# Kernel tuning notes

Hardware: AMD Instinct MI355X
Metric: run time of the kernel (lower is better)

Reference implementation:

```python
import jax, jax.numpy as jnp
import numpy as np
import math

T, C = 8192, 1024

def setup_inputs() -> dict:
    key = jax.random.key(0)
    ks = jax.random.split(key, 10)
    s = 1.0 / math.sqrt(C)
    return {
        "x": jax.random.normal(ks[0], (T, C), dtype=jnp.float32),
        "Wq": jax.random.normal(ks[1], (C, C), dtype=jnp.float32) * s,
        "bq": jax.random.normal(ks[2], (C,), dtype=jnp.float32) * s,
        "Wk": jax.random.normal(ks[3], (C, C), dtype=jnp.float32) * s,
        "bk": jax.random.normal(ks[4], (C,), dtype=jnp.float32) * s,
        "Wv": jax.random.normal(ks[5], (C, C), dtype=jnp.float32) * s,
        "bv": jax.random.normal(ks[6], (C,), dtype=jnp.float32) * s,
        "Wp": jax.random.normal(ks[7], (C, C), dtype=jnp.float32) * s,
        "bp": jax.random.normal(ks[8], (C,), dtype=jnp.float32) * s,
    }

def reference(x, Wq, bq, Wk, bk, Wv, bv, Wp, bp):
    # Single-head causal self-attention over an unbatched (T, C) sequence.
    t, c = x.shape
    q = x @ Wq.T + bq          # (T, C)
    k = x @ Wk.T + bk          # (T, C)
    v = x @ Wv.T + bv          # (T, C)
    att = (q @ k.T) / math.sqrt(c)                      # (T, T)
    causal = jnp.tril(jnp.ones((t, t), dtype=bool))
    att = jnp.where(causal, att, -jnp.inf)
    att = jax.nn.softmax(att, axis=-1)
    y = att @ v                                         # (T, C)
    y = y @ Wp.T + bp
    return y
```

## Files before the change

### kernel.cpp

```cpp
#include <hip/hip_runtime.h>
#include <hip/hip_bf16.h>

typedef __bf16 bf16x8 __attribute__((ext_vector_type(8)));
typedef float f32x4 __attribute__((ext_vector_type(4)));

static constexpr int Tn = 8192;
static constexpr int Cn = 1024;

#define DEVI __device__ __forceinline__

DEVI float bf2f(ushort u) { union { uint i; float f; } c; c.i = ((uint)u) << 16; return c.f; }
DEVI ushort f2bf(float f) {
  uint x = __builtin_bit_cast(uint, f);
  x += 0x7fffu + ((x >> 16) & 1u);
  return (ushort)(x >> 16);
}

typedef const __attribute__((address_space(1))) void glb_v;
typedef __attribute__((address_space(3))) void lds_v;

#define BAR()   __builtin_amdgcn_s_barrier()
#define SCH0()  __builtin_amdgcn_sched_barrier(0)
#define PRIO1() __builtin_amdgcn_s_setprio(1)
#define PRIO0() __builtin_amdgcn_s_setprio(0)

__global__ __launch_bounds__(256) void cast_all(
    const float* __restrict__ x, const float* __restrict__ wq, const float* __restrict__ wk,
    const float* __restrict__ wv, const float* __restrict__ wp,
    const float* __restrict__ bq, const float* __restrict__ bk, const float* __restrict__ bv,
    ushort* __restrict__ xb, ushort* __restrict__ wqkv, ushort* __restrict__ wpb,
    float* __restrict__ bqkv, float* __restrict__ lsum)
{
  const long long NX = (long long)Tn * Cn;
  const long long NW = (long long)Cn * Cn;
  if (blockIdx.x == 12291) {
    float4 z; z.x = z.y = z.z = z.w = 0.f;
#pragma unroll
    for (int j = 0; j < 8; ++j) ((float4*)lsum)[threadIdx.x * 8 + j] = z;
    return;
  }
  if (blockIdx.x >= 12288) {
    int id = ((blockIdx.x - 12288) * 256 + threadIdx.x) * 4;
#pragma unroll
    for (int e = 0; e < 4; ++e) {
      int j = id + e;
      if (j < 3 * Cn) bqkv[j] = j < Cn ? bq[j] : (j < 2 * Cn ? bk[j - Cn] : bv[j - 2 * Cn]);
    }
    return;
  }
  long long i = ((long long)blockIdx.x * 256 + threadIdx.x) * 4;
  const float* src; ushort* dst; long long off;
  if (i < NX) { src = x; dst = xb; off = i; }
  else {
    long long r = i - NX; int seg = (int)(r >> 20); off = r & (NW - 1);
    if (seg < 3) { src = seg == 0 ? wq : seg == 1 ? wk : wv; dst = wqkv + (size_t)seg * NW; }
    else         { src = wp; dst = wpb; }
  }
  float4 v = *reinterpret_cast<const float4*>(src + off);
  ushort4 o; o.x = f2bf(v.x); o.y = f2bf(v.y); o.z = f2bf(v.z); o.w = f2bf(v.w);
  *reinterpret_cast<ushort4*>(dst + off) = o;
}

template<bool OUT_BF16, bool HAS_BIAS, bool QKT, bool PVM, bool SPLIT3>
__global__ __launch_bounds__(256, 2)
void gemm_rp(const ushort* __restrict__ A, const ushort* __restrict__ Bt,
             const float* __restrict__ bias, void* __restrict__ outp,
             float* __restrict__ lsum,
             int K, int lda, int ldb, int ldc, float scale)
{
  __shared__ __align__(16) ushort sm[32768];

  const int tid = threadIdx.x, lane = tid & 63, wid = tid >> 6;
  const int wm = wid >> 1, wn = wid & 1;
  const int ln15 = lane & 15, lsec = lane >> 4;

  const int bx = blockIdx.x;
  int by = blockIdx.y;
  if (QKT && by < bx) return;
  if (PVM) by = (int)gridDim.y - 1 - by;
  const int rowA0 = by * 128, col0 = bx * 128;
  int NT = K >> 6;
  if (PVM) { int kl = (by + 1) * 128; if (kl < K) NT = kl >> 6; }

  const uint smb = (uint)(uintptr_t)&sm[0];

  auto stage = [&](int t, int b) {
    const int tt = t < NT ? t : NT - 1;
    const size_t k0 = (size_t)(tt << 6);
#pragma unroll
    for (int i = 0; i < 4; ++i) {
      int s = tid + i * 256; int row = s >> 3; int kcs = (s & 7) ^ (row & 7);
      const ushort* g = A + (size_t)(rowA0 + row) * (size_t)lda + k0 + kcs * 8;
      __builtin_amdgcn_global_load_lds((glb_v*)g, (lds_v*)(&sm[b * 16384 + s * 8]), 16, 0, 0);
    }
#pragma unroll
    for (int i = 0; i < 4; ++i) {
      int s = tid + i * 256; int row = s >> 3; int kcs = (s & 7) ^ (row & 7);
      const ushort* g = Bt + (size_t)(col0 + row) * (size_t)ldb + k0 + kcs * 8;
      __builtin_amdgcn_global_load_lds((glb_v*)g, (lds_v*)(&sm[b * 16384 + 8192 + s * 8]), 16, 0, 0);
    }
  };

  uint offA[2][4], offB[2][4];
#pragma unroll
  for (int ks = 0; ks < 2; ++ks) {
    int kc = ks * 4 + lsec;
#pragma unroll
    for (int mi = 0; mi < 4; ++mi) {
      int r = wm * 64 + mi * 16 + ln15;
      offA[ks][mi] = (uint)((r * 64 + (kc ^ (r & 7)) * 8) * 2);
    }
#pragma unroll
    for (int ni = 0; ni < 4; ++ni) {
      int c = wn * 64 + ni * 16 + ln15;
      offB[ks][ni] = (uint)(16384 + (c * 64 + (kc ^ (c & 7)) * 8) * 2);
    }
  }

  bf16x8 f0A[4], f0B[4], f1A[4], f1B[4];
  f32x4 acc[4][4] = {};

#define DSR(d, a) asm volatile("ds_read_b128 %0, %1" : "=v"(d) : "v"(a))
#define MMAC(FA, FB) { _Pragma("unroll") for (int mi = 0; mi < 4; ++mi) \
    _Pragma("unroll") for (int ni = 0; ni < 4; ++ni) \
      acc[mi][ni] = __builtin_amdgcn_mfma_f32_16x16x32_bf16(FA[mi], FB[ni], acc[mi][ni], 0, 0, 0); }

  stage(0, 0); stage(1, 1);
  asm volatile("s_waitcnt vmcnt(8)" ::: "memory");
  BAR();
  SCH0();
#pragma unroll
  for (int mi = 0; mi < 4; ++mi) DSR(f0A[mi], smb + offA[0][mi]);
#pragma unroll
  for (int ni = 0; ni < 4; ++ni) DSR(f0B[ni], smb + offB[0][ni]);
  SCH0();

  uint boff = 0;
  for (int t = 0; t < NT; ++t, boff ^= 32768u) {
#pragma unroll
    for (int mi = 0; mi < 4; ++mi) DSR(f1A[mi], smb + boff + offA[1][mi]);
#pragma unroll
    for (int ni = 0; ni < 4; ++ni) DSR(f1B[ni], smb + boff + offB[1][ni]);
    SCH0();
    asm volatile("s_waitcnt lgkmcnt(8)" ::: "memory");
    SCH0();
    PRIO1(); MMAC(f0A, f0B); PRIO0();
    SCH0();
    asm volatile("s_waitcnt lgkmcnt(0)" ::: "memory");
    BAR();
    stage(t + 2, t & 1);
    SCH0();
    asm volatile("s_waitcnt vmcnt(8)" ::: "memory");
    BAR();
    SCH0();
    const uint bo1 = boff ^ 32768u;
#pragma unroll
    for (int mi = 0; mi < 4; ++mi) DSR(f0A[mi], smb + bo1 + offA[0][mi]);
#pragma unroll
    for (int ni = 0; ni < 4; ++ni) DSR(f0B[ni], smb + bo1 + offB[0][ni]);
    SCH0();
    PRIO1(); MMAC(f1A, f1B); PRIO0();
    SCH0();
  }
  asm volatile("s_waitcnt vmcnt(0) lgkmcnt(0)" ::: "memory");
#undef DSR
#undef MMAC

  if constexpr (QKT) {
#pragma unroll
    for (int mi = 0; mi < 4; ++mi) {
#pragma unroll
      for (int j = 0; j < 4; ++j) {
        const int row = rowA0 + wm * 64 + mi * 16 + lsec * 4 + j;
        float rs = 0.f;
        ushort pb[4];
#pragma unroll
        for (int ni = 0; ni < 4; ++ni) {
          const int col = col0 + wn * 64 + ni * 16 + ln15;
          float p = 0.f;
          if (col <= row) p = __expf(acc[mi][ni][j] * scale);
          pb[ni] = f2bf(p);
          rs += bf2f(pb[ni]);
        }
#pragma unroll
        for (int o = 1; o < 16; o <<= 1) rs += __shfl_xor(rs, o);
        if (ln15 == 0) atomicAdd(&lsum[row], rs);
#pragma unroll
        for (int ni = 0; ni < 4; ++ni) {
          const int col = col0 + wn * 64 + ni * 16 + ln15;
          ((ushort*)outp)[(size_t)row * (size_t)ldc + col] = pb[ni];
        }
      }
    }
  } else {
#pragma unroll
    for (int mi = 0; mi < 4; ++mi) {
#pragma unroll
      for (int j = 0; j < 4; ++j) {
        const int row = rowA0 + wm * 64 + mi * 16 + lsec * 4 + j;
        float inv = 1.f;
        if constexpr (PVM) inv = 1.0f / lsum[row];
#pragma unroll
        for (int ni = 0; ni < 4; ++ni) {
          const int colg = col0 + wn * 64 + ni * 16 + ln15;
          float val = acc[mi][ni][j] * scale;
          if constexpr (PVM) val *= inv;
          if constexpr (HAS_BIAS) val += bias[colg];
          int col = colg; size_t segoff = 0;
          if constexpr (SPLIT3) { int seg = colg >> 10; col = colg & 1023; segoff = (size_t)seg * (size_t)Tn * Cn; }
          if constexpr (OUT_BF16) ((ushort*)outp)[segoff + (size_t)row * (size_t)ldc + col] = f2bf(val);
          else                    ((float*)outp)[segoff + (size_t)row * (size_t)ldc + col] = val;
        }
      }
    }
  }
}

__global__ __launch_bounds__(256) void transpose64(const ushort* __restrict__ in,
                                                   ushort* __restrict__ out,
                                                   int ldin, int ldout)
{
  __shared__ ushort tile[64][65];
  const int c0 = blockIdx.x * 64, r0 = blockIdx.y * 64;
  const int t = threadIdx.x;
#pragma unroll
  for (int i = t; i < 512; i += 256) {
    int r = i >> 3, kc = i & 7;
    uint4 v = *reinterpret_cast<const uint4*>(in + (size_t)(r0 + r) * ldin + c0 + kc * 8);
    const ushort* u = reinterpret_cast<const ushort*>(&v);
#pragma unroll
    for (int j = 0; j < 8; ++j) tile[r][kc * 8 + j] = u[j];
  }
  __syncthreads();
#pragma unroll
  for (int i = t; i < 512; i += 256) {
    int c = i >> 3, rc = i & 7;
    union { uint4 v; ushort u[8]; } pk;
#pragma unroll
    for (int j = 0; j < 8; ++j) pk.u[j] = tile[rc * 8 + j][c];
    *reinterpret_cast<uint4*>(out + (size_t)(c0 + c) * ldout + r0 + rc * 8) = pk.v;
  }
}

extern "C" void kernel_launch(void* const* d_in, const int* in_sizes, int n_in,
                              void* d_out, int out_size, void* d_ws, size_t ws_size,
                              hipStream_t stream)
{
  (void)in_sizes; (void)n_in; (void)out_size; (void)ws_size;
  const float* x  = (const float*)d_in[0];
  const float* Wq = (const float*)d_in[1];
  const float* bq = (const float*)d_in[2];
  const float* Wk = (const float*)d_in[3];
  const float* bk = (const float*)d_in[4];
  const float* Wv = (const float*)d_in[5];
  const float* bv = (const float*)d_in[6];
  const float* Wp = (const float*)d_in[7];
  const float* bp = (const float*)d_in[8];

  char* w = (char*)d_ws;
  const size_t TC = (size_t)Tn * Cn * 2, CC = (size_t)Cn * Cn * 2;
  ushort* xb   = (ushort*)w; w += TC;
  ushort* Wqkv = (ushort*)w; w += 3 * CC;
  ushort* wpb  = (ushort*)w; w += CC;
  float*  bqkv = (float*)w;  w += 16384;
  float*  lsum = (float*)w;  w += 32768;
  ushort* Qb   = (ushort*)w; w += TC;
  ushort* Kb   = (ushort*)w; w += TC;
  ushort* Vb   = (ushort*)w; w += TC;
  ushort* Vt   = (ushort*)w; w += TC;
  ushort* Yb   = (ushort*)w; w += TC;
  ushort* S    = (ushort*)w; w += (size_t)Tn * Tn * 2;

  cast_all<<<12292, 256, 0, stream>>>(x, Wq, Wk, Wv, Wp, bq, bk, bv,
                                      xb, Wqkv, wpb, bqkv, lsum);

  gemm_rp<true, true, false, false, true><<<dim3(24, 64), 256, 0, stream>>>(
      xb, Wqkv, bqkv, Qb, nullptr, Cn, Cn, Cn, Cn, 1.0f);

  transpose64<<<dim3(Cn / 64, Tn / 64), 256, 0, stream>>>(Vb, Vt, Cn, Tn);

  gemm_rp<true, false, true, false, false><<<dim3(64, 64), 256, 0, stream>>>(
      Qb, Kb, nullptr, S, lsum, Cn, Cn, Cn, Tn, 0.03125f);

  gemm_rp<true, false, false, true, false><<<dim3(8, 64), 256, 0, stream>>>(
      S, Vt, nullptr, Yb, lsum, Tn, Tn, Tn, Cn, 1.0f);

  gemm_rp<false, true, false, false, false><<<dim3(8, 64), 256, 0, stream>>>(
      Yb, wpb, bp, d_out, nullptr, Cn, Cn, Cn, Cn, 1.0f);
}
```

Baseline: 322.7 us.

## Triple-buffer LDS stages in GEMM mainloop and reorder QK^T block indexing

```diff
diff --git a/kernel.cpp b/kernel.cpp
--- a/kernel.cpp
+++ b/kernel.cpp
@@ -68,36 +68,41 @@
              float* __restrict__ lsum,
              int K, int lda, int ldb, int ldc, float scale)
 {
-  __shared__ __align__(16) ushort sm[32768];
+  __shared__ __align__(16) ushort sm[49152];
 
   const int tid = threadIdx.x, lane = tid & 63, wid = tid >> 6;
   const int wm = wid >> 1, wn = wid & 1;
   const int ln15 = lane & 15, lsec = lane >> 4;
 
-  const int bx = blockIdx.x;
-  int by = blockIdx.y;
-  if (QKT && by < bx) return;
-  if (PVM) by = (int)gridDim.y - 1 - by;
+  int bx, by;
+  if (QKT) {
+    by = blockIdx.x;
+    bx = blockIdx.y;
+    if (by < bx) return;
+  } else {
+    bx = blockIdx.x;
+    by = PVM ? ((int)gridDim.y - 1 - (int)blockIdx.y) : (int)blockIdx.y;
+  }
   const int rowA0 = by * 128, col0 = bx * 128;
   int NT = K >> 6;
   if (PVM) { int kl = (by + 1) * 128; if (kl < K) NT = kl >> 6; }
 
   const uint smb = (uint)(uintptr_t)&sm[0];
 
-  auto stage = [&](int t, int b) {
+  auto stage = [&](int t, uint eb) {
     const int tt = t < NT ? t : NT - 1;
     const size_t k0 = (size_t)(tt << 6);
 #pragma unroll
     for (int i = 0; i < 4; ++i) {
       int s = tid + i * 256; int row = s >> 3; int kcs = (s & 7) ^ (row & 7);
       const ushort* g = A + (size_t)(rowA0 + row) * (size_t)lda + k0 + kcs * 8;
-      __builtin_amdgcn_global_load_lds((glb_v*)g, (lds_v*)(&sm[b * 16384 + s * 8]), 16, 0, 0);
+      __builtin_amdgcn_global_load_lds((glb_v*)g, (lds_v*)(&sm[eb + s * 8]), 16, 0, 0);
     }
 #pragma unroll
     for (int i = 0; i < 4; ++i) {
       int s = tid + i * 256; int row = s >> 3; int kcs = (s & 7) ^ (row & 7);
       const ushort* g = Bt + (size_t)(col0 + row) * (size_t)ldb + k0 + kcs * 8;
-      __builtin_amdgcn_global_load_lds((glb_v*)g, (lds_v*)(&sm[b * 16384 + 8192 + s * 8]), 16, 0, 0);
+      __builtin_amdgcn_global_load_lds((glb_v*)g, (lds_v*)(&sm[eb + 8192 + s * 8]), 16, 0, 0);
     }
   };
 
@@ -125,8 +130,8 @@
     _Pragma("unroll") for (int ni = 0; ni < 4; ++ni) \
       acc[mi][ni] = __builtin_amdgcn_mfma_f32_16x16x32_bf16(FA[mi], FB[ni], acc[mi][ni], 0, 0, 0); }
 
-  stage(0, 0); stage(1, 1);
-  asm volatile("s_waitcnt vmcnt(8)" ::: "memory");
+  stage(0, 0); stage(1, 16384); stage(2, 32768);
+  asm volatile("s_waitcnt vmcnt(16)" ::: "memory");
   BAR();
   SCH0();
 #pragma unroll
@@ -135,12 +140,12 @@
   for (int ni = 0; ni < 4; ++ni) DSR(f0B[ni], smb + offB[0][ni]);
   SCH0();
 
-  uint boff = 0;
-  for (int t = 0; t < NT; ++t, boff ^= 32768u) {
-#pragma unroll
-    for (int mi = 0; mi < 4; ++mi) DSR(f1A[mi], smb + boff + offA[1][mi]);
-#pragma unroll
-    for (int ni = 0; ni < 4; ++ni) DSR(f1B[ni], smb + boff + offB[1][ni]);
+  uint bcur = 0;
+  for (int t = 0; t < NT; ++t) {
+#pragma unroll
+    for (int mi = 0; mi < 4; ++mi) DSR(f1A[mi], smb + bcur + offA[1][mi]);
+#pragma unroll
+    for (int ni = 0; ni < 4; ++ni) DSR(f1B[ni], smb + bcur + offB[1][ni]);
     SCH0();
     asm volatile("s_waitcnt lgkmcnt(8)" ::: "memory");
     SCH0();
@@ -148,19 +153,20 @@
     SCH0();
     asm volatile("s_waitcnt lgkmcnt(0)" ::: "memory");
     BAR();
-    stage(t + 2, t & 1);
-    SCH0();
-    asm volatile("s_waitcnt vmcnt(8)" ::: "memory");
+    stage(t + 3, bcur >> 1);
+    SCH0();
+    asm volatile("s_waitcnt vmcnt(16)" ::: "memory");
     BAR();
     SCH0();
-    const uint bo1 = boff ^ 32768u;
-#pragma unroll
-    for (int mi = 0; mi < 4; ++mi) DSR(f0A[mi], smb + bo1 + offA[0][mi]);
-#pragma unroll
-    for (int ni = 0; ni < 4; ++ni) DSR(f0B[ni], smb + bo1 + offB[0][ni]);
+    const uint bnext = (bcur == 65536u) ? 0u : bcur + 32768u;
+#pragma unroll
+    for (int mi = 0; mi < 4; ++mi) DSR(f0A[mi], smb + bnext + offA[0][mi]);
+#pragma unroll
+    for (int ni = 0; ni < 4; ++ni) DSR(f0B[ni], smb + bnext + offB[0][ni]);
     SCH0();
     PRIO1(); MMAC(f1A, f1B); PRIO0();
     SCH0();
+    bcur = bnext;
   }
   asm volatile("s_waitcnt vmcnt(0) lgkmcnt(0)" ::: "memory");
 #undef DSR
```

Result: slower. 382.1 us (+18.4%).

## Split-K the causal PV GEMM with atomic fp32 accumulation for load balance

Applied to the files above, without the earlier changes.

```diff
diff --git a/kernel.cpp b/kernel.cpp
--- a/kernel.cpp
+++ b/kernel.cpp
@@ -61,6 +61,31 @@
   *reinterpret_cast<ushort4*>(dst + off) = o;
 }
 
+__global__ __launch_bounds__(256) void zero_acc(float4* __restrict__ p)
+{
+  const int i = (blockIdx.x * 256 + threadIdx.x) * 4;
+  float4 z; z.x = z.y = z.z = z.w = 0.f;
+#pragma unroll
+  for (int j = 0; j < 4; ++j) p[i + j] = z;
+}
+
+__global__ __launch_bounds__(256) void ydiv(const float* __restrict__ Yacc,
+                                            const float* __restrict__ lsum,
+                                            ushort* __restrict__ Yb)
+{
+  const int i = (blockIdx.x * 256 + threadIdx.x) * 8;
+  const int row = i >> 10;
+  const float inv = 1.0f / lsum[row];
+  float4 a = *reinterpret_cast<const float4*>(Yacc + i);
+  float4 b = *reinterpret_cast<const float4*>(Yacc + i + 4);
+  union { uint4 v; ushort u[8]; } pk;
+  pk.u[0] = f2bf(a.x * inv); pk.u[1] = f2bf(a.y * inv);
+  pk.u[2] = f2bf(a.z * inv); pk.u[3] = f2bf(a.w * inv);
+  pk.u[4] = f2bf(b.x * inv); pk.u[5] = f2bf(b.y * inv);
+  pk.u[6] = f2bf(b.z * inv); pk.u[7] = f2bf(b.w * inv);
+  *reinterpret_cast<uint4*>(Yb + i) = pk.v;
+}
+
 template<bool OUT_BF16, bool HAS_BIAS, bool QKT, bool PVM, bool SPLIT3>
 __global__ __launch_bounds__(256, 2)
 void gemm_rp(const ushort* __restrict__ A, const ushort* __restrict__ Bt,
@@ -74,13 +99,26 @@
   const int wm = wid >> 1, wn = wid & 1;
   const int ln15 = lane & 15, lsec = lane >> 4;
 
-  const int bx = blockIdx.x;
-  int by = blockIdx.y;
-  if (QKT && by < bx) return;
-  if (PVM) by = (int)gridDim.y - 1 - by;
+  int bx, by;
+  if (QKT) {
+    by = blockIdx.x; bx = blockIdx.y;
+    if (by < bx) return;
+  } else {
+    bx = blockIdx.x; by = blockIdx.y;
+  }
   const int rowA0 = by * 128, col0 = bx * 128;
-  int NT = K >> 6;
-  if (PVM) { int kl = (by + 1) * 128; if (kl < K) NT = kl >> 6; }
+
+  int t0 = 0, NT = K >> 6;
+  if (PVM) {
+    int ktot = (by + 1) * 2;
+    if (ktot > (K >> 6)) ktot = K >> 6;
+    const int nz = (int)gridDim.z, bz = (int)blockIdx.z;
+    const int q = ktot / nz, r = ktot % nz;
+    const int len = q + (bz < r ? 1 : 0);
+    if (len == 0) return;
+    t0 = bz < r ? bz * (q + 1) : r * (q + 1) + (bz - r) * q;
+    NT = t0 + len;
+  }
 
   const uint smb = (uint)(uintptr_t)&sm[0];
 
@@ -125,7 +163,7 @@
     _Pragma("unroll") for (int ni = 0; ni < 4; ++ni) \
       acc[mi][ni] = __builtin_amdgcn_mfma_f32_16x16x32_bf16(FA[mi], FB[ni], acc[mi][ni], 0, 0, 0); }
 
-  stage(0, 0); stage(1, 1);
+  stage(t0, 0); stage(t0 + 1, 1);
   asm volatile("s_waitcnt vmcnt(8)" ::: "memory");
   BAR();
   SCH0();
@@ -136,7 +174,8 @@
   SCH0();
 
   uint boff = 0;
-  for (int t = 0; t < NT; ++t, boff ^= 32768u) {
+  const int len = NT - t0;
+  for (int it = 0; it < len; ++it, boff ^= 32768u) {
 #pragma unroll
     for (int mi = 0; mi < 4; ++mi) DSR(f1A[mi], smb + boff + offA[1][mi]);
 #pragma unroll
@@ -148,7 +187,7 @@
     SCH0();
     asm volatile("s_waitcnt lgkmcnt(0)" ::: "memory");
     BAR();
-    stage(t + 2, t & 1);
+    stage(t0 + it + 2, it & 1);
     SCH0();
     asm volatile("s_waitcnt vmcnt(8)" ::: "memory");
     BAR();
@@ -192,19 +231,30 @@
         }
       }
     }
-  } else {
+  } else if constexpr (PVM) {
+    float* Yacc = (float*)outp;
 #pragma unroll
     for (int mi = 0; mi < 4; ++mi) {
 #pragma unroll
       for (int j = 0; j < 4; ++j) {
         const int row = rowA0 + wm * 64 + mi * 16 + lsec * 4 + j;
-        float inv = 1.f;
-        if constexpr (PVM) inv = 1.0f / lsum[row];
+#pragma unroll
+        for (int ni = 0; ni < 4; ++ni) {
+          const int col = col0 + wn * 64 + ni * 16 + ln15;
+          atomicAdd(&Yacc[(size_t)row * (size_t)ldc + col], acc[mi][ni][j]);
+        }
+      }
+    }
+  } else {
+#pragma unroll
+    for (int mi = 0; mi < 4; ++mi) {
+#pragma unroll
+      for (int j = 0; j < 4; ++j) {
+        const int row = rowA0 + wm * 64 + mi * 16 + lsec * 4 + j;
 #pragma unroll
         for (int ni = 0; ni < 4; ++ni) {
           const int colg = col0 + wn * 64 + ni * 16 + ln15;
           float val = acc[mi][ni][j] * scale;
-          if constexpr (PVM) val *= inv;
           if constexpr (HAS_BIAS) val += bias[colg];
           int col = colg; size_t segoff = 0;
           if constexpr (SPLIT3) { int seg = colg >> 10; col = colg & 1023; segoff = (size_t)seg * (size_t)Tn * Cn; }
@@ -270,6 +320,7 @@
   ushort* Vt   = (ushort*)w; w += TC;
   ushort* Yb   = (ushort*)w; w += TC;
   ushort* S    = (ushort*)w; w += (size_t)Tn * Tn * 2;
+  float*  Yacc = (float*)Qb;
 
   cast_all<<<12292, 256, 0, stream>>>(x, Wq, Wk, Wv, Wp, bq, bk, bv,
                                       xb, Wqkv, wpb, bqkv, lsum);
@@ -282,8 +333,12 @@
   gemm_rp<true, false, true, false, false><<<dim3(64, 64), 256, 0, stream>>>(
       Qb, Kb, nullptr, S, lsum, Cn, Cn, Cn, Tn, 0.03125f);
 
-  gemm_rp<true, false, false, true, false><<<dim3(8, 64), 256, 0, stream>>>(
-      S, Vt, nullptr, Yb, lsum, Tn, Tn, Tn, Cn, 1.0f);
+  zero_acc<<<2048, 256, 0, stream>>>((float4*)Yacc);
+
+  gemm_rp<false, false, false, true, false><<<dim3(8, 64, 4), 256, 0, stream>>>(
+      S, Vt, nullptr, Yacc, nullptr, Tn, Tn, Tn, Cn, 1.0f);
+
+  ydiv<<<4096, 256, 0, stream>>>(Yacc, lsum, Yb);
 
   gemm_rp<false, true, false, false, false><<<dim3(8, 64), 256, 0, stream>>>(
       Yb, wpb, bp, d_out, nullptr, Cn, Cn, Cn, Cn, 1.0f);
```

New measurement: 368.0 us. 1.14x slower.
